# Kernel optimization log

Hardware: AMD Instinct MI355X
Metric: run time of the kernel (lower is better)

The kernel has to match this reference:

```python
import jax, jax.numpy as jnp
import numpy as np

P = 16; D = 256; NH = 8; L = 4; E = 8; K = 2; B = 32; IMG = 224; NC = 1000; FF = 4 * D
N = (IMG // P) ** 2  # 196 patches
HD = D // NH  # head dim
EPS = 1e-5


def setup_inputs():
    key = jax.random.key(0)
    ks = iter(jax.random.split(key, 16))
    s = 0.02  # init scale keeps softmax/logits well-conditioned
    rn = lambda shape: jax.random.normal(next(ks), shape, jnp.float32) * s
    return dict(
        x=jax.random.normal(next(ks), (B, 3, IMG, IMG), jnp.float32),
        patch_w=rn((3 * P * P, D)), patch_b=jnp.zeros((D,), jnp.float32),
        cls_token=rn((1, 1, D)), pos_embed=rn((1, N + 1, D)),
        router_w=rn((L, D, E)), router_b=jnp.zeros((L, E), jnp.float32),
        ln1_g=jnp.ones((L, E, D), jnp.float32), ln1_b=jnp.zeros((L, E, D), jnp.float32),
        qkv_w=rn((L, E, D, 3 * D)), qkv_b=jnp.zeros((L, E, 3 * D), jnp.float32),
        proj_w=rn((L, E, D, D)), proj_b=jnp.zeros((L, E, D), jnp.float32),
        ln2_g=jnp.ones((L, E, D), jnp.float32), ln2_b=jnp.zeros((L, E, D), jnp.float32),
        fc1_w=rn((L, E, D, FF)), fc1_b=jnp.zeros((L, E, FF), jnp.float32),
        fc2_w=rn((L, E, FF, D)), fc2_b=jnp.zeros((L, E, D), jnp.float32),
        norm_g=jnp.ones((D,), jnp.float32), norm_b=jnp.zeros((D,), jnp.float32),
        head_w=rn((D, NC)), head_b=jnp.zeros((NC,), jnp.float32),
    )


def _ln(x, g, b):
    m = x.mean(-1, keepdims=True)
    v = ((x - m) ** 2).mean(-1, keepdims=True)
    return (x - m) * jax.lax.rsqrt(v + EPS) * g + b


def _block(x, g1, b1, wqkv, bqkv, wp, bp, g2, b2, w1, bias1, w2, bias2):
    # standard ViT block: LN -> MHA -> residual, LN -> MLP(GELU) -> residual
    bsz, S, _ = x.shape
    h = _ln(x, g1, b1)
    qkv = (h @ wqkv + bqkv).reshape(bsz, S, 3, NH, HD)
    q, k, v = qkv[:, :, 0], qkv[:, :, 1], qkv[:, :, 2]  # [B,S,NH,HD]
    scores = jnp.einsum('bqhd,bkhd->bhqk', q, k) / np.float32(np.sqrt(HD))
    attn = jax.nn.softmax(scores, axis=-1)
    o = jnp.einsum('bhqk,bkhd->bqhd', attn, v).reshape(bsz, S, D)
    x = x + o @ wp + bp
    h2 = _ln(x, g2, b2)
    x = x + jax.nn.gelu(h2 @ w1 + bias1, approximate=False) @ w2 + bias2
    return x


def _moe_layer(x, rw, rb, g1, b1, wqkv, bqkv, wp, bp, g2, b2, w1, bias1, w2, bias2):
    probs = jax.nn.softmax(x @ rw + rb, axis=-1)            # [B,S,E]
    topv, topi = jax.lax.top_k(probs, K)                    # [B,S,K]
    topv = topv / topv.sum(-1, keepdims=True)
    # dense all-expert compute (faithful to source), vmapped over experts
    eo = jax.vmap(_block, in_axes=(None,) + (0,) * 12)(
        x, g1, b1, wqkv, bqkv, wp, bp, g2, b2, w1, bias1, w2, bias2)  # [E,B,S,D]
    eo = jnp.moveaxis(eo, 0, 2)                             # [B,S,E,D]
    sel = jnp.take_along_axis(eo, topi[..., None], axis=2)  # [B,S,K,D]
    return (sel * topv[..., None]).sum(axis=2)


def reference(x, patch_w, patch_b, cls_token, pos_embed, router_w, router_b,
              ln1_g, ln1_b, qkv_w, qkv_b, proj_w, proj_b, ln2_g, ln2_b,
              fc1_w, fc1_b, fc2_w, fc2_b, norm_g, norm_b, head_w, head_b):
    bsz = x.shape[0]
    g = IMG // P
    # patch embed: stride==kernel conv == patch extraction + matmul
    patches = x.reshape(bsz, 3, g, P, g, P).transpose(0, 2, 4, 1, 3, 5).reshape(bsz, N, 3 * P * P)
    h = patches @ patch_w + patch_b                          # [B,N,D]
    cls = jnp.broadcast_to(cls_token, (bsz, 1, D))
    h = jnp.concatenate([cls, h], axis=1) + pos_embed        # [B,N+1,D]
    for l in range(L):
        h = _moe_layer(h, router_w[l], router_b[l], ln1_g[l], ln1_b[l],
                       qkv_w[l], qkv_b[l], proj_w[l], proj_b[l], ln2_g[l], ln2_b[l],
                       fc1_w[l], fc1_b[l], fc2_w[l], fc2_b[l])
    h = _ln(h, norm_g, norm_b)
    return h[:, 0] @ head_w + head_b                         # [B,NC]
```

## Files before the change

### kernel.cpp

```cpp
#include <hip/hip_runtime.h>
#include <math.h>

#define SEQ 197
#define BATCH 32
#define DIM 256
#define NHEAD 8
#define HDIM 32
#define NEXP 8
#define NLAYER 4
#define FFDIM 1024
#define NCLS 1000
#define NPATCH 196
#define TOK (BATCH * SEQ)
#define CAP 13120
#define YB 99
#define KT 64

__device__ __forceinline__ void gload16(const float* g, float* l) {
  __builtin_amdgcn_global_load_lds(
      (const __attribute__((address_space(1))) void*)g,
      (__attribute__((address_space(3))) void*)l, 16, 0, 0);
}

__global__ __launch_bounds__(256) void k_im2col(const float* __restrict__ x,
                                                float* __restrict__ Apat) {
  int idx = blockIdx.x * 256 + threadIdx.x;
  if (idx >= BATCH * NPATCH * 768) return;
  int cpp = idx % 768;
  int m = idx / 768;
  int n = m % NPATCH;
  int b = m / NPATCH;
  int c = cpp >> 8;
  int py = (cpp >> 4) & 15;
  int px = cpp & 15;
  int gy = n / 14, gx = n % 14;
  Apat[idx] = x[(((size_t)b * 3 + c) * 224 + gy * 16 + py) * 224 + gx * 16 + px];
}

__global__ __launch_bounds__(256) void k_foldw(const float* __restrict__ qw,
                                               const float* __restrict__ g1,
                                               float* __restrict__ w4) {
  size_t idx = (size_t)blockIdx.x * 256 + threadIdx.x;
  if (idx >= (size_t)32 * 256 * 768) return;
  size_t kn = idx % (256 * 768);
  int le = (int)(idx / (256 * 768));
  int k = (int)(kn / 768);
  w4[idx] = qw[idx] * g1[le * 256 + k];
}

__global__ __launch_bounds__(256) void k_foldb(const float* __restrict__ qw,
                                               const float* __restrict__ qb,
                                               const float* __restrict__ b1,
                                               float* __restrict__ b4) {
  int le = blockIdx.y;
  int col = blockIdx.x * 256 + threadIdx.x;
  const float* w = qw + (size_t)le * 256 * 768 + col;
  const float* lb = b1 + (size_t)le * 256;
  float acc = 0.f;
  for (int k = 0; k < 256; ++k) acc = fmaf(lb[k], w[(size_t)k * 768], acc);
  b4[(size_t)le * 768 + col] = acc + qb[(size_t)le * 768 + col];
}

__global__ __launch_bounds__(256) void k_gemm_t(
    const float* __restrict__ A, const float* __restrict__ W,
    const float* __restrict__ bias, const float* __restrict__ R,
    const float* __restrict__ X2, const float* __restrict__ PW,
    const int* __restrict__ ptok, const int* __restrict__ off_e,
    const int* __restrict__ cnt_e, float* __restrict__ out, int M, int N,
    int K, int Wld, int wcol, int bstride, int ebase, int mode, int flags) {
  __shared__ float As[2][16][68];
  __shared__ float Bs[2][16][128];
  int gx = gridDim.x, gy = gridDim.y;
  int nwg = gx * gy * gridDim.z;
  int lin = blockIdx.x + gx * (blockIdx.y + gy * blockIdx.z);
  int q8 = nwg >> 3, r8 = nwg & 7;
  int xcd = lin & 7, jj0 = lin >> 3;
  int nlin = (xcd < r8 ? xcd * (q8 + 1) : r8 * (q8 + 1) + (xcd - r8) * q8) + jj0;
  int bx = nlin % gx;
  int t1 = nlin / gx;
  int by = t1 % gy;
  int bz = t1 / gy;

  int e = ebase + bz;
  bool seg = (flags & 1) != 0;
  int rows = seg ? cnt_e[e] : M;
  int row0 = by * 64;
  if (row0 >= rows) return;
  int col0 = bx * 128;
  int tid = threadIdx.x;
  int base = seg ? off_e[e] : 0;
  const float* Wp = W + (size_t)e * K * Wld + wcol;
  const float* bp = bias + (size_t)e * bstride + wcol;

  int rr = tid >> 2, kq = (tid & 3) * 4;
  int r = row0 + rr;
  bool val = r < rows;
  int rc = val ? r : rows - 1;
  int gr0 = base + rc;
  int arow = seg ? ((flags & 2) ? ptok[gr0] : gr0) : rc;
  const float* aptr = A + (size_t)arow * K + kq;
  float msk = val ? 1.f : 0.f;
  int wv = tid >> 6, lane = tid & 63;
  const float* bsrc0 =
      Wp + (size_t)(2 * wv + (lane >> 5)) * Wld + col0 + (lane & 31) * 4;
  const float* bsrc1 = bsrc0 + (size_t)8 * Wld;

  gload16(bsrc0, &Bs[0][2 * wv][0]);
  gload16(bsrc1, &Bs[0][8 + 2 * wv][0]);
  {
    float4 av = *(const float4*)aptr;
    As[0][kq + 0][rr] = av.x * msk;
    As[0][kq + 1][rr] = av.y * msk;
    As[0][kq + 2][rr] = av.z * msk;
    As[0][kq + 3][rr] = av.w * msk;
  }
  __syncthreads();

  int tx = tid & 15, ty = tid >> 4;
  float acc0[4][4] = {};
  float acc1[4][4] = {};
  int cur = 0;
  for (int k0 = 0; k0 < K; k0 += 16) {
    int nb = cur ^ 1;
    bool more = (k0 + 16) < K;
    float4 av;
    if (more) {
      av = *(const float4*)(aptr + k0 + 16);
      gload16(bsrc0 + (size_t)(k0 + 16) * Wld, &Bs[nb][2 * wv][0]);
      gload16(bsrc1 + (size_t)(k0 + 16) * Wld, &Bs[nb][8 + 2 * wv][0]);
    }
#pragma unroll
    for (int k = 0; k < 16; ++k) {
      float4 a = *(const float4*)&As[cur][k][ty * 4];
      float4 b0 = *(const float4*)&Bs[cur][k][tx * 4];
      float4 b1 = *(const float4*)&Bs[cur][k][64 + tx * 4];
      float aa[4] = {a.x, a.y, a.z, a.w};
      float b0a[4] = {b0.x, b0.y, b0.z, b0.w};
      float b1a[4] = {b1.x, b1.y, b1.z, b1.w};
#pragma unroll
      for (int i = 0; i < 4; ++i)
#pragma unroll
        for (int j = 0; j < 4; ++j) {
          acc0[i][j] = fmaf(aa[i], b0a[j], acc0[i][j]);
          acc1[i][j] = fmaf(aa[i], b1a[j], acc1[i][j]);
        }
    }
    if (more) {
      As[nb][kq + 0][rr] = av.x * msk;
      As[nb][kq + 1][rr] = av.y * msk;
      As[nb][kq + 2][rr] = av.z * msk;
      As[nb][kq + 3][rr] = av.w * msk;
    }
    __syncthreads();
    cur = nb;
  }
#pragma unroll
  for (int i = 0; i < 4; ++i) {
    int rrow = row0 + ty * 4 + i;
    if (rrow >= rows) continue;
    int gr = base + rrow;
#pragma unroll
    for (int c = 0; c < 2; ++c) {
#pragma unroll
      for (int j = 0; j < 4; ++j) {
        int col = col0 + c * 64 + tx * 4 + j;
        float v = (c ? acc1[i][j] : acc0[i][j]) + bp[col];
        if (mode == 0) {
          size_t orow = seg ? (size_t)gr : (size_t)bz * M + rrow;
          out[orow * N + col] = v;
        } else if (mode == 1) {
          int t = ptok[gr];
          out[(size_t)gr * N + col] = v + R[(size_t)t * N + col];
        } else if (mode == 2) {
          out[(size_t)gr * N + col] =
              0.5f * v * (1.f + erff(v * 0.70710678118654752f));
        } else {
          int t = ptok[gr];
          atomicAdd(&out[(size_t)t * N + col],
                    PW[gr] * (X2[(size_t)gr * N + col] + v));
        }
      }
    }
  }
}

__global__ __launch_bounds__(128) void k_gemm8(
    const float* __restrict__ A, const float* __restrict__ W,
    const float* __restrict__ bias, const float* __restrict__ R,
    const float* __restrict__ X2, const float* __restrict__ PW,
    const int* __restrict__ ptok, const int* __restrict__ off_e,
    const int* __restrict__ cnt_e, float* __restrict__ out, int M, int N,
    int K, int Wld, int wcol, int bstride, int ebase, int mode, int flags) {
  __shared__ float As[2][64][16];
  __shared__ float Bs[2][16][128];
  int gx = gridDim.x, gy = gridDim.y;
  int nwg = gx * gy * gridDim.z;
  int lin = blockIdx.x + gx * (blockIdx.y + gy * blockIdx.z);
  int q8 = nwg >> 3, r8 = nwg & 7;
  int xcd = lin & 7, jj0 = lin >> 3;
  int nlin = (xcd < r8 ? xcd * (q8 + 1) : r8 * (q8 + 1) + (xcd - r8) * q8) + jj0;
  int bx = nlin % gx;
  int t1 = nlin / gx;
  int by = t1 % gy;
  int bz = t1 / gy;

  int e = ebase + bz;
  bool seg = (flags & 1) != 0;
  int rows = seg ? cnt_e[e] : M;
  int row0 = by * 64;
  if (row0 >= rows) return;
  int col0 = bx * 128;
  int tid = threadIdx.x;
  int wv = tid >> 6, lane = tid & 63;
  int base = seg ? off_e[e] : 0;
  const float* Wp = W + (size_t)e * K * Wld + wcol;
  const float* bp = bias + (size_t)e * bstride + wcol;

  const float* pA0;
  const float* pA1;
  {
    int l4 = lane >> 2, lk = (lane & 3) * 4;
#pragma unroll
    for (int c = 0; c < 2; ++c) {
      int r = row0 + wv * 32 + c * 16 + l4;
      int rc = r < rows ? r : rows - 1;
      int gr0 = base + rc;
      int arow = seg ? ((flags & 2) ? ptok[gr0] : gr0) : rc;
      const float* p = A + (size_t)arow * K + lk;
      if (c == 0) pA0 = p; else pA1 = p;
    }
  }
  const float* pB = Wp + (size_t)(lane >> 5) * Wld + col0 + (lane & 31) * 4;

  gload16(pA0, &As[0][wv * 32][0]);
  gload16(pA1, &As[0][wv * 32 + 16][0]);
#pragma unroll
  for (int c = 0; c < 4; ++c) {
    int rb = 2 * (wv * 4 + c);
    gload16(pB + (size_t)rb * Wld, &Bs[0][rb][0]);
  }
  __syncthreads();

  int tx = tid & 15, ty = tid >> 4;
  float acc0[8][4] = {};
  float acc1[8][4] = {};
  int cur = 0;
  for (int k0 = 0; k0 < K; k0 += 16) {
    int nb = cur ^ 1;
    bool more = (k0 + 16) < K;
    if (more) {
      gload16(pA0 + k0 + 16, &As[nb][wv * 32][0]);
      gload16(pA1 + k0 + 16, &As[nb][wv * 32 + 16][0]);
#pragma unroll
      for (int c = 0; c < 4; ++c) {
        int rb = 2 * (wv * 4 + c);
        gload16(pB + (size_t)(k0 + 16 + rb) * Wld, &Bs[nb][rb][0]);
      }
    }
#pragma unroll
    for (int k4 = 0; k4 < 4; ++k4) {
      float areg[8][4];
#pragma unroll
      for (int i = 0; i < 8; ++i) {
        float4 t = *(const float4*)&As[cur][ty + 8 * i][k4 * 4];
        areg[i][0] = t.x;
        areg[i][1] = t.y;
        areg[i][2] = t.z;
        areg[i][3] = t.w;
      }
#pragma unroll
      for (int kk = 0; kk < 4; ++kk) {
        float4 b0 = *(const float4*)&Bs[cur][k4 * 4 + kk][tx * 4];
        float4 b1 = *(const float4*)&Bs[cur][k4 * 4 + kk][64 + tx * 4];
        float b0a[4] = {b0.x, b0.y, b0.z, b0.w};
        float b1a[4] = {b1.x, b1.y, b1.z, b1.w};
#pragma unroll
        for (int i = 0; i < 8; ++i) {
          float av = areg[i][kk];
#pragma unroll
          for (int j = 0; j < 4; ++j) {
            acc0[i][j] = fmaf(av, b0a[j], acc0[i][j]);
            acc1[i][j] = fmaf(av, b1a[j], acc1[i][j]);
          }
        }
      }
    }
    __syncthreads();
    cur = nb;
  }
#pragma unroll
  for (int i = 0; i < 8; ++i) {
    int rrow = row0 + ty + 8 * i;
    if (rrow >= rows) continue;
    int gr = base + rrow;
#pragma unroll
    for (int c = 0; c < 2; ++c) {
#pragma unroll
      for (int j = 0; j < 4; ++j) {
        int col = col0 + c * 64 + tx * 4 + j;
        float v = (c ? acc1[i][j] : acc0[i][j]) + bp[col];
        if (mode == 0) {
          size_t orow = seg ? (size_t)gr : (size_t)bz * M + rrow;
          out[orow * N + col] = v;
        } else if (mode == 1) {
          int t = ptok[gr];
          out[(size_t)gr * N + col] = v + R[(size_t)t * N + col];
        } else if (mode == 2) {
          out[(size_t)gr * N + col] =
              0.5f * v * (1.f + erff(v * 0.70710678118654752f));
        } else {
          int t = ptok[gr];
          atomicAdd(&out[(size_t)t * N + col],
                    PW[gr] * (X2[(size_t)gr * N + col] + v));
        }
      }
    }
  }
}

__global__ __launch_bounds__(256) void k_assemble(const float* __restrict__ tmp,
                                                  const float* __restrict__ cls,
                                                  const float* __restrict__ pos,
                                                  float* __restrict__ h) {
  int idx = blockIdx.x * 256 + threadIdx.x;
  if (idx >= TOK * DIM) return;
  int d = idx & 255;
  int t = idx >> 8;
  int s = t % SEQ;
  int b = t / SEQ;
  float v = (s == 0) ? cls[d] : tmp[((size_t)b * NPATCH + s - 1) * DIM + d];
  h[idx] = v + pos[s * DIM + d];
}

__global__ __launch_bounds__(64) void k_router(
    const float* __restrict__ h, const float* __restrict__ rw,
    const float* __restrict__ rb, int* __restrict__ cnt_eb,
    int* __restrict__ tmp_s, float* __restrict__ tmp_w) {
  int t = blockIdx.x;
  int lane = threadIdx.x;
  float hv[4];
  const float* hp = h + (size_t)t * DIM + lane * 4;
#pragma unroll
  for (int i = 0; i < 4; i++) hv[i] = hp[i];
  float lg[8];
#pragma unroll
  for (int e = 0; e < 8; e++) {
    float p = 0.f;
#pragma unroll
    for (int i = 0; i < 4; i++) p = fmaf(hv[i], rw[(lane * 4 + i) * 8 + e], p);
#pragma unroll
    for (int off = 32; off; off >>= 1) p += __shfl_down(p, off);
    lg[e] = p;
  }
  if (lane == 0) {
#pragma unroll
    for (int e = 0; e < 8; e++) lg[e] += rb[e];
    float mx = lg[0];
#pragma unroll
    for (int e = 1; e < 8; e++) mx = fmaxf(mx, lg[e]);
    float pr[8];
#pragma unroll
    for (int e = 0; e < 8; e++) pr[e] = expf(lg[e] - mx);
    int i0 = 0;
#pragma unroll
    for (int e = 1; e < 8; e++)
      if (pr[e] > pr[i0]) i0 = e;
    int i1 = -1;
#pragma unroll
    for (int e = 0; e < 8; e++)
      if (e != i0 && (i1 < 0 || pr[e] > pr[i1])) i1 = e;
    float wsum = pr[i0] + pr[i1];
    int b = t / SEQ, s = t - b * SEQ;
    int eb0 = i0 * 32 + b;
    int p0 = atomicAdd(&cnt_eb[eb0], 1);
    tmp_s[eb0 * SEQ + p0] = s;
    tmp_w[eb0 * SEQ + p0] = pr[i0] / wsum;
    int eb1 = i1 * 32 + b;
    int p1 = atomicAdd(&cnt_eb[eb1], 1);
    tmp_s[eb1 * SEQ + p1] = s;
    tmp_w[eb1 * SEQ + p1] = pr[i1] / wsum;
  }
}

__global__ __launch_bounds__(64) void k_scan(const int* __restrict__ cnt_eb,
                                             int* __restrict__ off_eb,
                                             int* __restrict__ off_e,
                                             int* __restrict__ cnt_e) {
  if (threadIdx.x == 0 && blockIdx.x == 0) {
    int g = 0;
    for (int e = 0; e < 8; e++) {
      off_e[e] = g;
      int ce = 0;
      for (int b = 0; b < 32; b++) {
        off_eb[e * 32 + b] = g + ce;
        ce += cnt_eb[e * 32 + b];
      }
      cnt_e[e] = ce;
      g += (ce + 63) & ~63;
    }
  }
}

__global__ __launch_bounds__(256) void k_scatter(
    const int* __restrict__ cnt_eb, const int* __restrict__ off_eb,
    const int* __restrict__ tmp_s, const float* __restrict__ tmp_w,
    int* __restrict__ ptok, float* __restrict__ pw) {
  int eb = blockIdx.x;
  int b = eb & 31;
  int c = cnt_eb[eb];
  int o = off_eb[eb];
  for (int i = threadIdx.x; i < c; i += 256) {
    ptok[o + i] = b * SEQ + tmp_s[eb * SEQ + i];
    pw[o + i] = tmp_w[eb * SEQ + i];
  }
}

__global__ __launch_bounds__(256) void k_ln_noaff(const float* __restrict__ X,
                                                  float* __restrict__ Y) {
  int t = blockIdx.x;
  int d = threadIdx.x;
  float v = X[(size_t)t * DIM + d];
  __shared__ float red[4];
  float s = v;
#pragma unroll
  for (int o = 32; o; o >>= 1) s += __shfl_down(s, o);
  if ((d & 63) == 0) red[d >> 6] = s;
  __syncthreads();
  float mean = (red[0] + red[1] + red[2] + red[3]) * (1.f / 256.f);
  __syncthreads();
  float c = v - mean;
  float s2 = c * c;
#pragma unroll
  for (int o = 32; o; o >>= 1) s2 += __shfl_down(s2, o);
  if ((d & 63) == 0) red[d >> 6] = s2;
  __syncthreads();
  float var = (red[0] + red[1] + red[2] + red[3]) * (1.f / 256.f);
  Y[(size_t)t * DIM + d] = c * rsqrtf(var + 1e-5f);
}

__global__ __launch_bounds__(256) void k_ln_seg(
    const float* __restrict__ X, const float* __restrict__ g,
    const float* __restrict__ bta, float* __restrict__ Y,
    const int* __restrict__ off_e, const int* __restrict__ cnt_e) {
  int e = blockIdx.y;
  int cnt = cnt_e[e];
  int base = off_e[e];
  int d = threadIdx.x;
  float gv = g[e * DIM + d];
  float bv = bta[e * DIM + d];
  __shared__ float red[4];
  for (int r = blockIdx.x; r < cnt; r += gridDim.x) {
    size_t gr = (size_t)(base + r);
    float v = X[gr * DIM + d];
    float s = v;
#pragma unroll
    for (int o = 32; o; o >>= 1) s += __shfl_down(s, o);
    if ((d & 63) == 0) red[d >> 6] = s;
    __syncthreads();
    float mean = (red[0] + red[1] + red[2] + red[3]) * (1.f / 256.f);
    __syncthreads();
    float c = v - mean;
    float s2 = c * c;
#pragma unroll
    for (int o = 32; o; o >>= 1) s2 += __shfl_down(s2, o);
    if ((d & 63) == 0) red[d >> 6] = s2;
    __syncthreads();
    float var = (red[0] + red[1] + red[2] + red[3]) * (1.f / 256.f);
    Y[gr * DIM + d] = c * rsqrtf(var + 1e-5f) * gv + bv;
    __syncthreads();
  }
}

__global__ __launch_bounds__(256) void k_attn(
    const float* __restrict__ qc, const float* __restrict__ kv,
    float* __restrict__ oc, const int* __restrict__ cnt_eb,
    const int* __restrict__ off_eb, int ebase) {
  int bx = blockIdx.x;
  int hh = bx & 7;
  int b = (bx >> 3) & 31;
  int ez = bx >> 8;
  int eb = (ebase + ez) * 32 + b;
  int cnt = cnt_eb[eb];
  if (cnt == 0) return;
  int off = off_eb[eb];
  __shared__ float Ks[KT][HDIM];
  __shared__ float Vs[KT][HDIM];
  const float* base = kv + ((size_t)ez * TOK + (size_t)b * SEQ) * 512;
  int tid = threadIdx.x;
  int grp = tid >> 2;
  int ln = tid & 3;
  int nrounds = (cnt + 63) >> 6;
  for (int qr = 0; qr < nrounds; ++qr) {
    int qi = qr * 64 + grp;
    bool act = qi < cnt;
    int qc_i = act ? qi : cnt - 1;
    const float* qp = qc + (size_t)(off + qc_i) * DIM + hh * HDIM + ln * 8;
    float4 q0 = *(const float4*)qp;
    float4 q1 = *(const float4*)(qp + 4);
    float qv[8] = {q0.x, q0.y, q0.z, q0.w, q1.x, q1.y, q1.z, q1.w};
    float m = -1e30f, l = 0.f;
    float acc[8] = {};
    for (int t0 = 0; t0 < SEQ; t0 += KT) {
      int nk = (SEQ - t0) < KT ? (SEQ - t0) : KT;
      __syncthreads();
      for (int i = tid; i < nk * 16; i += 256) {
        int row = i >> 4, half = (i >> 3) & 1, c4 = (i & 7) * 4;
        const float* p =
            base + (size_t)(t0 + row) * 512 + half * 256 + hh * HDIM + c4;
        if (half == 0)
          *(float4*)&Ks[row][c4] = *(const float4*)p;
        else
          *(float4*)&Vs[row][c4] = *(const float4*)p;
      }
      __syncthreads();
      const float* KsL = &Ks[0][ln * 8];
      const float* VsL = &Vs[0][ln * 8];
#pragma unroll 2
      for (int j = 0; j < nk; ++j) {
        const float4* kr = (const float4*)(KsL + j * HDIM);
        float4 k0 = kr[0], k1 = kr[1];
        float s = qv[0] * k0.x;
        s = fmaf(qv[1], k0.y, s);
        s = fmaf(qv[2], k0.z, s);
        s = fmaf(qv[3], k0.w, s);
        s = fmaf(qv[4], k1.x, s);
        s = fmaf(qv[5], k1.y, s);
        s = fmaf(qv[6], k1.z, s);
        s = fmaf(qv[7], k1.w, s);
        s += __shfl_xor(s, 1);
        s += __shfl_xor(s, 2);
        s *= 0.17677669529663687f;
        float nm = fmaxf(m, s);
        float f = expf(m - nm);
        float e2 = expf(s - nm);
        m = nm;
        l = fmaf(l, f, e2);
        const float4* vr = (const float4*)(VsL + j * HDIM);
        float4 v0 = vr[0], v1 = vr[1];
        acc[0] = fmaf(acc[0], f, e2 * v0.x);
        acc[1] = fmaf(acc[1], f, e2 * v0.y);
        acc[2] = fmaf(acc[2], f, e2 * v0.z);
        acc[3] = fmaf(acc[3], f, e2 * v0.w);
        acc[4] = fmaf(acc[4], f, e2 * v1.x);
        acc[5] = fmaf(acc[5], f, e2 * v1.y);
        acc[6] = fmaf(acc[6], f, e2 * v1.z);
        acc[7] = fmaf(acc[7], f, e2 * v1.w);
      }
    }
    if (act) {
      float inv = 1.f / l;
      float* op = oc + (size_t)(off + qi) * DIM + hh * HDIM + ln * 8;
      float4 o0 = {acc[0] * inv, acc[1] * inv, acc[2] * inv, acc[3] * inv};
      float4 o1 = {acc[4] * inv, acc[5] * inv, acc[6] * inv, acc[7] * inv};
      *(float4*)op = o0;
      *(float4*)(op + 4) = o1;
    }
  }
}

__global__ __launch_bounds__(256) void k_head(const float* __restrict__ h,
                                              const float* __restrict__ ng,
                                              const float* __restrict__ nb,
                                              const float* __restrict__ hw,
                                              const float* __restrict__ hb,
                                              float* __restrict__ out) {
  int b = blockIdx.x;
  int d = threadIdx.x;
  float v = h[(size_t)b * SEQ * DIM + d];
  __shared__ float red[4];
  __shared__ float hls[DIM];
  float s = v;
#pragma unroll
  for (int off = 32; off; off >>= 1) s += __shfl_down(s, off);
  if ((d & 63) == 0) red[d >> 6] = s;
  __syncthreads();
  float mean = (red[0] + red[1] + red[2] + red[3]) * (1.f / 256.f);
  __syncthreads();
  float c = v - mean;
  float s2 = c * c;
#pragma unroll
  for (int off = 32; off; off >>= 1) s2 += __shfl_down(s2, off);
  if ((d & 63) == 0) red[d >> 6] = s2;
  __syncthreads();
  float var = (red[0] + red[1] + red[2] + red[3]) * (1.f / 256.f);
  hls[d] = c * rsqrtf(var + 1e-5f) * ng[d] + nb[d];
  __syncthreads();
  for (int j = d; j < NCLS; j += 256) {
    float sdot = hb[j];
    for (int k2 = 0; k2 < DIM; k2++)
      sdot = fmaf(hls[k2], hw[(size_t)k2 * NCLS + j], sdot);
    out[(size_t)b * NCLS + j] = sdot;
  }
}

extern "C" void kernel_launch(void* const* d_in, const int* in_sizes, int n_in,
                              void* d_out, int out_size, void* d_ws,
                              size_t ws_size, hipStream_t stream) {
  const float* x = (const float*)d_in[0];
  const float* patch_w = (const float*)d_in[1];
  const float* patch_b = (const float*)d_in[2];
  const float* cls_token = (const float*)d_in[3];
  const float* pos_embed = (const float*)d_in[4];
  const float* router_w = (const float*)d_in[5];
  const float* router_b = (const float*)d_in[6];
  const float* ln1_g = (const float*)d_in[7];
  const float* ln1_b = (const float*)d_in[8];
  const float* qkv_w = (const float*)d_in[9];
  const float* qkv_b = (const float*)d_in[10];
  const float* proj_w = (const float*)d_in[11];
  const float* proj_b = (const float*)d_in[12];
  const float* ln2_g = (const float*)d_in[13];
  const float* ln2_b = (const float*)d_in[14];
  const float* fc1_w = (const float*)d_in[15];
  const float* fc1_b = (const float*)d_in[16];
  const float* fc2_w = (const float*)d_in[17];
  const float* fc2_b = (const float*)d_in[18];
  const float* norm_g = (const float*)d_in[19];
  const float* norm_b = (const float*)d_in[20];
  const float* head_w = (const float*)d_in[21];
  const float* head_b = (const float*)d_in[22];

  float* ws = (float*)d_ws;
  size_t off = 0;
  float* xhat = ws + off; off += (size_t)TOK * DIM;
  float* hbuf = ws + off; off += (size_t)TOK * DIM;
  float* accb = ws + off; off += (size_t)TOK * DIM;
  float* qc   = ws + off; off += (size_t)CAP * DIM;
  float* oc   = ws + off; off += (size_t)CAP * DIM;
  float* x2c  = ws + off; off += (size_t)CAP * DIM;
  float* ffc  = ws + off; off += (size_t)CAP * FFDIM;
  float* w4   = ws + off; off += (size_t)32 * DIM * 768;
  float* b4   = ws + off; off += (size_t)32 * 768;
  float* pwb  = ws + off; off += CAP;
  float* tmpw = ws + off; off += 256 * SEQ;
  int* ptok   = (int*)(ws + off); off += CAP;
  int* tmps   = (int*)(ws + off); off += 256 * SEQ;
  int* cnt_eb = (int*)(ws + off); off += 256;
  int* off_eb = (int*)(ws + off); off += 256;
  int* off_e  = (int*)(ws + off); off += 8;
  int* cnt_e  = (int*)(ws + off); off += 8;
  float* kv4 = ffc;
  float* hlnc = qc;

  k_foldw<<<(32 * 256 * 768 + 255) / 256, 256, 0, stream>>>(qkv_w, ln1_g, w4);
  k_foldb<<<dim3(3, 32), 256, 0, stream>>>(qkv_w, qkv_b, ln1_b, b4);

  int tot = BATCH * NPATCH * 768;
  k_im2col<<<(tot + 255) / 256, 256, 0, stream>>>(x, ffc);
  k_gemm_t<<<dim3(2, 98, 1), 256, 0, stream>>>(
      ffc, patch_w, patch_b, nullptr, nullptr, nullptr, nullptr, nullptr,
      nullptr, qc, BATCH * NPATCH, DIM, 768, DIM, 0, 0, 0, 0, 0);
  k_assemble<<<(TOK * DIM + 255) / 256, 256, 0, stream>>>(qc, cls_token,
                                                          pos_embed, hbuf);

  float* h = hbuf;
  float* acc = accb;
  for (int l = 0; l < NLAYER; ++l) {
    hipMemsetAsync(acc, 0, (size_t)TOK * DIM * sizeof(float), stream);
    hipMemsetAsync(cnt_eb, 0, 256 * sizeof(int), stream);
    k_router<<<TOK, 64, 0, stream>>>(h, router_w + (size_t)l * DIM * NEXP,
                                     router_b + (size_t)l * NEXP, cnt_eb, tmps,
                                     tmpw);
    k_scan<<<1, 64, 0, stream>>>(cnt_eb, off_eb, off_e, cnt_e);
    k_scatter<<<256, 256, 0, stream>>>(cnt_eb, off_eb, tmps, tmpw, ptok, pwb);
    k_ln_noaff<<<TOK, 256, 0, stream>>>(h, xhat);

    const float* Wl = w4 + (size_t)l * NEXP * DIM * 768;
    const float* Bl = b4 + (size_t)l * NEXP * 768;

    k_gemm_t<<<dim3(2, YB, 8), 256, 0, stream>>>(
        xhat, Wl, Bl, nullptr, nullptr, nullptr, ptok, off_e, cnt_e, qc, 0,
        DIM, DIM, 768, 0, 768, 0, 0, 3);

    for (int grp = 0; grp < 2; ++grp) {
      int eb0 = grp * 4;
      k_gemm8<<<dim3(4, YB, 4), 128, 0, stream>>>(
          xhat, Wl, Bl, nullptr, nullptr, nullptr, nullptr, nullptr, nullptr,
          kv4, TOK, 512, DIM, 768, 256, 768, eb0, 0, 0);
      k_attn<<<1024, 256, 0, stream>>>(qc, kv4, oc, cnt_eb, off_eb, eb0);
    }

    k_gemm_t<<<dim3(2, YB, 8), 256, 0, stream>>>(
        oc, proj_w + (size_t)l * NEXP * DIM * DIM,
        proj_b + (size_t)l * NEXP * DIM, h, nullptr, nullptr, ptok, off_e,
        cnt_e, x2c, 0, DIM, DIM, DIM, 0, DIM, 0, 1, 1);
    k_ln_seg<<<dim3(YB, 8), 256, 0, stream>>>(
        x2c, ln2_g + (size_t)l * NEXP * DIM, ln2_b + (size_t)l * NEXP * DIM,
        hlnc, off_e, cnt_e);
    k_gemm8<<<dim3(8, YB, 8), 128, 0, stream>>>(
        hlnc, fc1_w + (size_t)l * NEXP * DIM * FFDIM,
        fc1_b + (size_t)l * NEXP * FFDIM, nullptr, nullptr, nullptr, ptok,
        off_e, cnt_e, ffc, 0, FFDIM, DIM, FFDIM, 0, FFDIM, 0, 2, 1);
    k_gemm8<<<dim3(2, YB, 8), 128, 0, stream>>>(
        ffc, fc2_w + (size_t)l * NEXP * FFDIM * DIM,
        fc2_b + (size_t)l * NEXP * DIM, nullptr, x2c, pwb, ptok, off_e, cnt_e,
        acc, 0, DIM, FFDIM, DIM, 0, DIM, 0, 3, 1);
    float* t = h;
    h = acc;
    acc = t;
  }
  k_head<<<BATCH, 256, 0, stream>>>(h, norm_g, norm_b, head_w, head_b,
                                    (float*)d_out);
}
```

Baseline: 3.744 ms.

## Enlarge expert GEMM tile to 128x128 with 256 threads, rebalance kernel choices

```diff
diff --git a/kernel.cpp b/kernel.cpp
--- a/kernel.cpp
+++ b/kernel.cpp
@@ -14,6 +14,7 @@
 #define TOK (BATCH * SEQ)
 #define CAP 13120
 #define YB 99
+#define YB128 50
 #define KT 64
 
 __device__ __forceinline__ void gload16(const float* g, float* l) {
@@ -184,14 +185,14 @@
   }
 }
 
-__global__ __launch_bounds__(128) void k_gemm8(
+__global__ __launch_bounds__(256) void k_gemm16(
     const float* __restrict__ A, const float* __restrict__ W,
     const float* __restrict__ bias, const float* __restrict__ R,
     const float* __restrict__ X2, const float* __restrict__ PW,
     const int* __restrict__ ptok, const int* __restrict__ off_e,
     const int* __restrict__ cnt_e, float* __restrict__ out, int M, int N,
     int K, int Wld, int wcol, int bstride, int ebase, int mode, int flags) {
-  __shared__ float As[2][64][16];
+  __shared__ float As[2][128][16];
   __shared__ float Bs[2][16][128];
   int gx = gridDim.x, gy = gridDim.y;
   int nwg = gx * gy * gridDim.z;
@@ -207,7 +208,7 @@
   int e = ebase + bz;
   bool seg = (flags & 1) != 0;
   int rows = seg ? cnt_e[e] : M;
-  int row0 = by * 64;
+  int row0 = by * 128;
   if (row0 >= rows) return;
   int col0 = bx * 128;
   int tid = threadIdx.x;
@@ -230,15 +231,13 @@
       if (c == 0) pA0 = p; else pA1 = p;
     }
   }
-  const float* pB = Wp + (size_t)(lane >> 5) * Wld + col0 + (lane & 31) * 4;
+  const float* pB = Wp + (size_t)(4 * wv + (lane >> 5)) * Wld + col0 +
+                    (lane & 31) * 4;
 
   gload16(pA0, &As[0][wv * 32][0]);
   gload16(pA1, &As[0][wv * 32 + 16][0]);
-#pragma unroll
-  for (int c = 0; c < 4; ++c) {
-    int rb = 2 * (wv * 4 + c);
-    gload16(pB + (size_t)rb * Wld, &Bs[0][rb][0]);
-  }
+  gload16(pB, &Bs[0][4 * wv][0]);
+  gload16(pB + (size_t)2 * Wld, &Bs[0][4 * wv + 2][0]);
   __syncthreads();
 
   int tx = tid & 15, ty = tid >> 4;
@@ -251,22 +250,19 @@
     if (more) {
       gload16(pA0 + k0 + 16, &As[nb][wv * 32][0]);
       gload16(pA1 + k0 + 16, &As[nb][wv * 32 + 16][0]);
-#pragma unroll
-      for (int c = 0; c < 4; ++c) {
-        int rb = 2 * (wv * 4 + c);
-        gload16(pB + (size_t)(k0 + 16 + rb) * Wld, &Bs[nb][rb][0]);
-      }
+      gload16(pB + (size_t)(k0 + 16) * Wld, &Bs[nb][4 * wv][0]);
+      gload16(pB + (size_t)(k0 + 18) * Wld, &Bs[nb][4 * wv + 2][0]);
     }
 #pragma unroll
     for (int k4 = 0; k4 < 4; ++k4) {
-      float areg[8][4];
+      float a[8][4];
 #pragma unroll
       for (int i = 0; i < 8; ++i) {
-        float4 t = *(const float4*)&As[cur][ty + 8 * i][k4 * 4];
-        areg[i][0] = t.x;
-        areg[i][1] = t.y;
-        areg[i][2] = t.z;
-        areg[i][3] = t.w;
+        float4 t = *(const float4*)&As[cur][ty + 16 * i][k4 * 4];
+        a[i][0] = t.x;
+        a[i][1] = t.y;
+        a[i][2] = t.z;
+        a[i][3] = t.w;
       }
 #pragma unroll
       for (int kk = 0; kk < 4; ++kk) {
@@ -276,7 +272,7 @@
         float b1a[4] = {b1.x, b1.y, b1.z, b1.w};
 #pragma unroll
         for (int i = 0; i < 8; ++i) {
-          float av = areg[i][kk];
+          float av = a[i][kk];
 #pragma unroll
           for (int j = 0; j < 4; ++j) {
             acc0[i][j] = fmaf(av, b0a[j], acc0[i][j]);
@@ -290,7 +286,7 @@
   }
 #pragma unroll
   for (int i = 0; i < 8; ++i) {
-    int rrow = row0 + ty + 8 * i;
+    int rrow = row0 + ty + 16 * i;
     if (rrow >= rows) continue;
     int gr = base + rrow;
 #pragma unroll
@@ -647,7 +643,7 @@
 
   int tot = BATCH * NPATCH * 768;
   k_im2col<<<(tot + 255) / 256, 256, 0, stream>>>(x, ffc);
-  k_gemm_t<<<dim3(2, 98, 1), 256, 0, stream>>>(
+  k_gemm16<<<dim3(2, 49, 1), 256, 0, stream>>>(
       ffc, patch_w, patch_b, nullptr, nullptr, nullptr, nullptr, nullptr,
       nullptr, qc, BATCH * NPATCH, DIM, 768, DIM, 0, 0, 0, 0, 0);
   k_assemble<<<(TOK * DIM + 255) / 256, 256, 0, stream>>>(qc, cls_token,
@@ -674,7 +670,7 @@
 
     for (int grp = 0; grp < 2; ++grp) {
       int eb0 = grp * 4;
-      k_gemm8<<<dim3(4, YB, 4), 128, 0, stream>>>(
+      k_gemm16<<<dim3(4, YB128, 4), 256, 0, stream>>>(
           xhat, Wl, Bl, nullptr, nullptr, nullptr, nullptr, nullptr, nullptr,
           kv4, TOK, 512, DIM, 768, 256, 768, eb0, 0, 0);
       k_attn<<<1024, 256, 0, stream>>>(qc, kv4, oc, cnt_eb, off_eb, eb0);
@@ -687,11 +683,11 @@
     k_ln_seg<<<dim3(YB, 8), 256, 0, stream>>>(
         x2c, ln2_g + (size_t)l * NEXP * DIM, ln2_b + (size_t)l * NEXP * DIM,
         hlnc, off_e, cnt_e);
-    k_gemm8<<<dim3(8, YB, 8), 128, 0, stream>>>(
+    k_gemm16<<<dim3(8, YB128, 8), 256, 0, stream>>>(
         hlnc, fc1_w + (size_t)l * NEXP * DIM * FFDIM,
         fc1_b + (size_t)l * NEXP * FFDIM, nullptr, nullptr, nullptr, ptok,
         off_e, cnt_e, ffc, 0, FFDIM, DIM, FFDIM, 0, FFDIM, 0, 2, 1);
-    k_gemm8<<<dim3(2, YB, 8), 128, 0, stream>>>(
+    k_gemm_t<<<dim3(2, YB, 8), 256, 0, stream>>>(
         ffc, fc2_w + (size_t)l * NEXP * FFDIM * DIM,
         fc2_b + (size_t)l * NEXP * DIM, nullptr, x2c, pwb, ptok, off_e, cnt_e,
         acc, 0, DIM, FFDIM, DIM, 0, DIM, 0, 3, 1);
```

Result: faster. 3.350 ms (-10.5%).
